# Optimization experiments

Measured on AMD Instinct MI355X. Metric: run time of the kernel, lower is better.

## Reference

```python
import jax, jax.numpy as jnp
import numpy as np

HEAD_NUM = 16

def setup_inputs() -> dict:
    key = jax.random.key(0)
    k1, k2 = jax.random.split(key)
    bs, seq, d = 2, 2048, 1024
    embeddings = jax.random.normal(k1, (bs, seq, d), dtype=jnp.float32)
    W = jax.random.normal(k2, (d, 3 * d), dtype=jnp.float32) * (1.0 / np.sqrt(d))
    b = jnp.zeros((3 * d,), dtype=jnp.float32)
    return {"embeddings": embeddings, "W": W, "b": b}

def reference(embeddings, W, b):
    bs, seq, d = embeddings.shape
    h = HEAD_NUM
    qkv = embeddings @ W + b                      # [b, s, 3d]
    q, k, v = jnp.split(qkv, 3, axis=-1)          # each [b, s, d]
    hd = d // h
    # Faithful to source: reshape to (bs, seq, head_dim, heads) then permute
    def split_heads(x, head_dim):
        return x.reshape(bs, seq, head_dim, h).transpose(0, 3, 1, 2)  # [b, h, s, hd]
    mq = split_heads(q, hd)
    mk = split_heads(k, hd)
    mv = split_heads(v, hd)
    scale = jnp.sqrt(jnp.asarray(hd, dtype=mq.dtype))
    scores = jnp.einsum('bhqd,bhkd->bhqk', mq, mk) / scale  # [b, h, s, s]
    attn = jax.nn.softmax(scores, axis=-1)
    out = jnp.einsum('bhqk,bhkv->bhqv', attn, mv)            # [b, h, s, hd]
    return out.transpose(0, 2, 1, 3).reshape(bs, seq, -1)    # [b, s, d]
```

## Files before the change

### kernel.cpp

```cpp
#include <hip/hip_runtime.h>
#include <stdint.h>

typedef unsigned short u16;
typedef unsigned int u32;
typedef float f32x4 __attribute__((ext_vector_type(4)));
typedef __bf16 bf16x8 __attribute__((ext_vector_type(8)));

#define BS 2
#define SEQ 2048
#define DIM 1024
#define NW3 3072
#define NH 16
#define HD 64

#define MFMA_BF16(a, b, c) __builtin_amdgcn_mfma_f32_16x16x32_bf16((a), (b), (c), 0, 0, 0)

#define GLL16(g, l)                                                                \
  __builtin_amdgcn_global_load_lds(                                                \
      (__attribute__((address_space(1))) void*)(void*)(uintptr_t)(g),              \
      (__attribute__((address_space(3))) void*)(l), 16, 0, 0)

__device__ __forceinline__ float fexp2(float x) {
#if defined(__has_builtin)
#if __has_builtin(__builtin_amdgcn_exp2f)
  return __builtin_amdgcn_exp2f(x);
#else
  return exp2f(x);
#endif
#else
  return exp2f(x);
#endif
}

__device__ __forceinline__ u16 f2bf(float x) {
  __bf16 h = (__bf16)x;
  return __builtin_bit_cast(u16, h);
}

#define CSC 0.18033688011112042f

__global__ __launch_bounds__(256) void conv_kernel(const float* __restrict__ A,
                                                   u16* __restrict__ O,
                                                   const float* __restrict__ W,
                                                   u16* __restrict__ Wt) {
  if (blockIdx.x < 4096) {
    int i = (blockIdx.x * 256 + threadIdx.x) * 4;
    float4 v = *(const float4*)(A + i);
    union { u16 u[4]; ushort4 v4; } p;
    p.u[0] = f2bf(v.x); p.u[1] = f2bf(v.y); p.u[2] = f2bf(v.z); p.u[3] = f2bf(v.w);
    *(ushort4*)(O + i) = p.v4;
  } else {
    int id = (blockIdx.x - 4096) * 256 + threadIdx.x;
    int kc = id / NW3;
    int n = id - kc * NW3;
    union { u16 u[8]; uint4 v; } p;
#pragma unroll
    for (int i = 0; i < 8; ++i) p.u[i] = f2bf(W[(kc * 8 + i) * NW3 + n]);
    int h = n & 15, hd = (n & 1023) >> 4;
    int np = (n & ~1023) + h * 64 + hd;
    *(uint4*)(Wt + np * DIM + kc * 8) = p.v;
  }
}

#define GSTAGE(ADST, BDST, KT)                                                 \
  {                                                                            \
    const int koff = (KT) * 64;                                \
    _Pragma("unroll") for (int r = 0; r < 2; ++r) {                            \
      int l = r * 256 + t;                            \
      int row = l >> 2, pos = l & 3;                                           \
      int kc = pos ^ (row & 3);                                                \
      GLL16(Abase + row * 2048 + koff + kc * 16, (char*)(ADST) + l * 16);      \
      GLL16(Bbase + row * 2048 + koff + kc * 16, (char*)(BDST) + l * 16);      \
    }                                                                          \
  }

#define GCOMPUTE(AT, BT)                                                       \
  {                                                                            \
    bf16x8 af[4], bfr[4];                                                      \
    _Pragma("unroll") for (int mt = 0; mt < 4; ++mt) {                         \
      int row = wm + mt * 16 + c;                                              \
      int kc = quad ^ (row & 3);                                               \
      af[mt] = *(const bf16x8*)((const char*)(AT) + row * 64 + kc * 16);       \
    }                                                                          \
    _Pragma("unroll") for (int nt = 0; nt < 4; ++nt) {                         \
      int row = wn + nt * 16 + c;                                              \
      int kc = quad ^ (row & 3);                                               \
      bfr[nt] = *(const bf16x8*)((const char*)(BT) + row * 64 + kc * 16);      \
    }                                                                          \
    _Pragma("unroll") for (int mt = 0; mt < 4; ++mt)                           \
      _Pragma("unroll") for (int nt = 0; nt < 4; ++nt)                         \
        acc[mt][nt] = MFMA_BF16(af[mt], bfr[nt], acc[mt][nt]);                 \
  }

__global__ __launch_bounds__(256) void gemm_qkv_kernel(
    const u16* __restrict__ Ab, const u16* __restrict__ Bt, const float* __restrict__ bias,
    u16* __restrict__ Q, u16* __restrict__ K, u16* __restrict__ Vt) {
  __shared__ __align__(16) u16 Aa[128 * 32];
  __shared__ __align__(16) u16 Ab2[128 * 32];
  __shared__ __align__(16) u16 Ba[128 * 32];
  __shared__ __align__(16) u16 Bb2[128 * 32];
  const int t = threadIdx.x;
  const int lane = t & 63, wave = t >> 6;
  const int c = lane & 15, quad = lane >> 4;
  const int tm = blockIdx.x / 24, tn = blockIdx.x - tm * 24;
  const int wm = (wave >> 1) * 64, wn = (wave & 1) * 64;

  const char* Abase = (const char*)(Ab + (size_t)tm * 128 * DIM);
  const char* Bbase = (const char*)(Bt + (size_t)tn * 128 * DIM);

  f32x4 z = {0.f, 0.f, 0.f, 0.f};
  f32x4 acc[4][4];
#pragma unroll
  for (int i = 0; i < 4; ++i)
#pragma unroll
    for (int j = 0; j < 4; ++j) acc[i][j] = z;

  GSTAGE(Aa, Ba, 0);
  __syncthreads();
  for (int kt = 0; kt < 32; kt += 2) {
    GSTAGE(Ab2, Bb2, kt + 1);
    GCOMPUTE(Aa, Ba);
    __syncthreads();
    if (kt + 2 < 32) GSTAGE(Aa, Ba, kt + 2);
    GCOMPUTE(Ab2, Bb2);
    __syncthreads();
  }

#pragma unroll
  for (int nt = 0; nt < 4; ++nt) {
    int np = tn * 128 + wn + nt * 16 + c;
    int which = np >> 10;
    int rem = np & 1023;
    int h = rem >> 6, hd = rem & 63;
    float bv = bias[(np & ~1023) + hd * 16 + h];
    float sc = (which == 0) ? CSC : 1.0f;
    float bvs = bv * sc;
#pragma unroll
    for (int mt = 0; mt < 4; ++mt) {
      int mbase = tm * 128 + wm + mt * 16 + quad * 4;
      int bI = mbase >> 11;
      int s0 = mbase & 2047;
      if (which == 2) {
        union { u16 u[4]; uint2 v; } p;
#pragma unroll
        for (int r = 0; r < 4; ++r) p.u[r] = f2bf(acc[mt][nt][r] + bv);
        *(uint2*)(Vt + ((size_t)(bI * NH + h) * HD + hd) * SEQ + s0) = p.v;
      } else {
        u16* dst = (which == 0) ? Q : K;
#pragma unroll
        for (int r = 0; r < 4; ++r)
          dst[((size_t)(bI * NH + h) * SEQ + (s0 + r)) * HD + hd] =
              f2bf(acc[mt][nt][r] * sc + bvs);
      }
    }
  }
}

#define STAGE_KV(KDST, VDST, KTILE)                                            \
  {                                                                            \
    const char* Ktb = Kb + (size_t)(KTILE) * 8192;        \
    const char* Vtb = Vb + (size_t)(KTILE) * 128;         \
    _Pragma("unroll") for (int r = 0; r < 2; ++r) {                            \
      int l = r * 256 + t;                                                     \
      int row = l >> 3, pos = l & 7;                                           \
      int kc = pos ^ (row & 7);                                                \
      GLL16(Ktb + row * 128 + kc * 16, (char*)(KDST) + l * 16);                \
      GLL16(Vtb + row * 4096 + kc * 16, (char*)(VDST) + l * 16);               \
    }                                                                          \
  }

#define COMPUTE_TILE(KT, VT)                                                   \
  {                                                                            \
    f32x4 sT[2][2]; \
    sT[0][0] = z; sT[0][1] = z; sT[1][0] = z; sT[1][1] = z;                    \
    _Pragma("unroll") for (int mt2 = 0; mt2 < 2; ++mt2) {                      \
      _Pragma("unroll") for (int ks = 0; ks < 2; ++ks) {                       \
        int row = ws * 32 + mt2 * 16 + c;                                      \
        int kc = (ks * 4 + quad) ^ (row & 7);                                  \
        bf16x8 kf = *(const bf16x8*)((const char*)(KT) + row * 128 + kc * 16); \
        sT[mt2][0] = MFMA_BF16(kf, qf[0][ks], sT[mt2][0]);                     \
        sT[mt2][1] = MFMA_BF16(kf, qf[1][ks], sT[mt2][1]);                     \
      }                                                                        \
    }                                                                          \
    bf16x8 pf[2];                                                              \
    _Pragma("unroll") for (int nt = 0; nt < 2; ++nt) {                         \
      u32 pk[2][2];                                                            \
      _Pragma("unroll") for (int mt2 = 0; mt2 < 2; ++mt2) {                    \
        float p0 = fexp2(sT[mt2][nt][0]);                                      \
        float p1 = fexp2(sT[mt2][nt][1]);                                      \
        float p2 = fexp2(sT[mt2][nt][2]);                                      \
        float p3 = fexp2(sT[mt2][nt][3]);                                      \
        smA[nt] += p0 + p1; smB[nt] += p2 + p3;                                \
        pk[mt2][0] = (u32)f2bf(p0) | ((u32)f2bf(p1) << 16);                    \
        pk[mt2][1] = (u32)f2bf(p2) | ((u32)f2bf(p3) << 16);                    \
      }                                                                        \
      u32 a0 = __shfl(pk[0][0], sl0), a1 = __shfl(pk[0][1], sl0);              \
      u32 a2 = __shfl(pk[0][0], sl1), a3 = __shfl(pk[0][1], sl1);              \
      u32 b0 = __shfl(pk[1][0], sl0), b1 = __shfl(pk[1][1], sl0);              \
      u32 b2 = __shfl(pk[1][0], sl1), b3 = __shfl(pk[1][1], sl1);              \
      uint4 wv;                                                                \
      wv.x = hi ? b0 : a0; wv.y = hi ? b1 : a1;                                \
      wv.z = hi ? b2 : a2; wv.w = hi ? b3 : a3;                                \
      pf[nt] = __builtin_bit_cast(bf16x8, wv);                                 \
    }                                                                          \
    _Pragma("unroll") for (int mt = 0; mt < 4; ++mt) {                         \
      int row = mt * 16 + c;                                                   \
      int kc = vq ^ (row & 7);                                                 \
      bf16x8 vf = *(const bf16x8*)((const char*)(VT) + row * 128 + kc * 16);   \
      accO[mt][0] = MFMA_BF16(vf, pf[0], accO[mt][0]);                         \
      accO[mt][1] = MFMA_BF16(vf, pf[1], accO[mt][1]);                         \
    }                                                                          \
  }

__global__ __launch_bounds__(256, 4) void attn_kernel(
    const u16* __restrict__ Q, const u16* __restrict__ K,
    const u16* __restrict__ Vt, float* __restrict__ Out) {
  __shared__ __align__(16) u16 Ka[64 * 64];
  __shared__ __align__(16) u16 Kb2[64 * 64];
  __shared__ __align__(16) u16 Va[64 * 64];
  __shared__ __align__(16) u16 Vb2[64 * 64];
  const int t = threadIdx.x;
  const int lane = t & 63, wave = t >> 6;
  const int c = lane & 15, quad = lane >> 4;
  const int wq = wave & 1, ws = wave >> 1;
  const int qt = blockIdx.x & 31, bh = blockIdx.x >> 5;
  const int h = bh & 15, b = bh >> 4;

  const u16* Qb = Q + ((size_t)bh * SEQ + qt * 64) * HD;
  const char* Kb = (const char*)(K + (size_t)bh * SEQ * HD);
  const char* Vb = (const char*)(Vt + (size_t)bh * HD * SEQ);

#pragma unroll
  for (int r = 0; r < 2; ++r) {
    int l = r * 256 + t;
    int row = l >> 3, pos = l & 7;
    int kc = pos ^ (row & 7);
    GLL16((const char*)Qb + row * 128 + kc * 16, (char*)Ka + l * 16);
  }
  __syncthreads();
  bf16x8 qf[2][2];
#pragma unroll
  for (int nt = 0; nt < 2; ++nt)
#pragma unroll
    for (int ks = 0; ks < 2; ++ks) {
      int row = wq * 32 + nt * 16 + c;
      int kc = (ks * 4 + quad) ^ (row & 7);
      qf[nt][ks] = *(const bf16x8*)((const char*)Ka + row * 128 + kc * 16);
    }
  __syncthreads();

  float smA[2] = {0.f, 0.f}, smB[2] = {0.f, 0.f};
  f32x4 z = {0.f, 0.f, 0.f, 0.f};
  f32x4 accO[4][2];
#pragma unroll
  for (int i = 0; i < 4; ++i) { accO[i][0] = z; accO[i][1] = z; }

  const int sl0 = c + 16 * ((quad & 1) * 2);
  const int sl1 = sl0 + 16;
  const bool hi = quad >= 2;
  const int vq = ws * 4 + quad;

  STAGE_KV(Ka, Va, 0);
  __syncthreads();

  for (int kt = 0; kt < 32; kt += 2) {
    STAGE_KV(Kb2, Vb2, kt + 1);
    COMPUTE_TILE(Ka, Va);
    __syncthreads();
    if (kt + 2 < 32) STAGE_KV(Ka, Va, kt + 2);
    COMPUTE_TILE(Kb2, Vb2);
    __syncthreads();
  }

  float sm[2];
#pragma unroll
  for (int nt = 0; nt < 2; ++nt) {
    float s = smA[nt] + smB[nt];
    s += __shfl_xor(s, 16);
    s += __shfl_xor(s, 32);
    sm[nt] = s;
  }
  if (ws == 1) {
    float* fb = (float*)(wq ? (void*)Kb2 : (void*)Ka);
#pragma unroll
    for (int mt = 0; mt < 4; ++mt)
#pragma unroll
      for (int nt = 0; nt < 2; ++nt)
        *(f32x4*)(fb + (mt * 2 + nt) * 256 + lane * 4) = accO[mt][nt];
    float* lb = (float*)Va + wq * 128;
    lb[lane * 2] = sm[0];
    lb[lane * 2 + 1] = sm[1];
  }
  __syncthreads();
  if (ws == 0) {
    const float* fb = (const float*)(wq ? (void*)Kb2 : (void*)Ka);
#pragma unroll
    for (int mt = 0; mt < 4; ++mt)
#pragma unroll
      for (int nt = 0; nt < 2; ++nt)
        accO[mt][nt] += *(const f32x4*)(fb + (mt * 2 + nt) * 256 + lane * 4);
    const float* lb = (const float*)Va + wq * 128;
    float inv0 = 1.f / (sm[0] + lb[lane * 2]);
    float inv1 = 1.f / (sm[1] + lb[lane * 2 + 1]);
    int s0 = qt * 64 + wq * 32 + c;
#pragma unroll
    for (int mt = 0; mt < 4; ++mt) {
#pragma unroll
      for (int nt = 0; nt < 2; ++nt) {
        float inv = nt ? inv1 : inv0;
        float4 o;
        o.x = accO[mt][nt][0] * inv;
        o.y = accO[mt][nt][1] * inv;
        o.z = accO[mt][nt][2] * inv;
        o.w = accO[mt][nt][3] * inv;
        size_t off = ((size_t)(b * SEQ + s0 + nt * 16)) * DIM + h * HD + mt * 16 + quad * 4;
        *(float4*)(Out + off) = o;
      }
    }
  }
}

extern "C" void kernel_launch(void* const* d_in, const int* in_sizes, int n_in,
                              void* d_out, int out_size, void* d_ws, size_t ws_size,
                              hipStream_t stream) {
  (void)in_sizes; (void)n_in; (void)out_size; (void)ws_size;
  const float* emb = (const float*)d_in[0];
  const float* W = (const float*)d_in[1];
  const float* bias = (const float*)d_in[2];
  float* out = (float*)d_out;
  char* ws = (char*)d_ws;
  u16* Ab = (u16*)ws;
  u16* Wt = (u16*)(ws + 8388608);
  u16* Qd = (u16*)(ws + 14680064);
  u16* Kd = (u16*)(ws + 23068672);
  u16* Vd = (u16*)(ws + 31457280);

  conv_kernel<<<5632, 256, 0, stream>>>(emb, Ab, W, Wt);
  gemm_qkv_kernel<<<768, 256, 0, stream>>>(Ab, Wt, bias, Qd, Kd, Vd);
  attn_kernel<<<1024, 256, 0, stream>>>(Qd, Kd, Vd, out);
}
```

Before: 175.6 us.

## Triple-buffer K/V tiles with one barrier per tile, XCD-aware block mapping, setprio

The attention loop moves from double-buffered K/V staging with two full syncthreads per tile pair to a rotating triple buffer. Loads run two tiles ahead and each tile waits on a partial vmcnt before a single barrier. Blocks are remapped so that all query tiles of a head land on the same XCD, so K/V reuse stays in that XCD's L2. MFMA sections are wrapped in s_setprio to favour matrix issue. The cost is 50% more LDS per block (24KB), which may limit occupancy, plus hand-tuned waitcnt values that must match the load counts exactly.

```diff
diff --git a/kernel.cpp b/kernel.cpp
--- a/kernel.cpp
+++ b/kernel.cpp
@@ -173,6 +173,7 @@
   {                                                                            \
     f32x4 sT[2][2]; \
     sT[0][0] = z; sT[0][1] = z; sT[1][0] = z; sT[1][1] = z;                    \
+    __builtin_amdgcn_s_setprio(1);                                             \
     _Pragma("unroll") for (int mt2 = 0; mt2 < 2; ++mt2) {                      \
       _Pragma("unroll") for (int ks = 0; ks < 2; ++ks) {                       \
         int row = ws * 32 + mt2 * 16 + c;                                      \
@@ -182,6 +183,7 @@
         sT[mt2][1] = MFMA_BF16(kf, qf[1][ks], sT[mt2][1]);                     \
       }                                                                        \
     }                                                                          \
+    __builtin_amdgcn_s_setprio(0);                                             \
     bf16x8 pf[2];                                                              \
     _Pragma("unroll") for (int nt = 0; nt < 2; ++nt) {                         \
       u32 pk[2][2];                                                            \
@@ -203,6 +205,7 @@
       wv.z = hi ? b2 : a2; wv.w = hi ? b3 : a3;                                \
       pf[nt] = __builtin_bit_cast(bf16x8, wv);                                 \
     }                                                                          \
+    __builtin_amdgcn_s_setprio(1);                                             \
     _Pragma("unroll") for (int mt = 0; mt < 4; ++mt) {                         \
       int row = mt * 16 + c;                                                   \
       int kc = vq ^ (row & 7);                                                 \
@@ -210,20 +213,26 @@
       accO[mt][0] = MFMA_BF16(vf, pf[0], accO[mt][0]);                         \
       accO[mt][1] = MFMA_BF16(vf, pf[1], accO[mt][1]);                         \
     }                                                                          \
+    __builtin_amdgcn_s_setprio(0);                                             \
   }
 
 __global__ __launch_bounds__(256, 4) void attn_kernel(
     const u16* __restrict__ Q, const u16* __restrict__ K,
     const u16* __restrict__ Vt, float* __restrict__ Out) {
-  __shared__ __align__(16) u16 Ka[64 * 64];
-  __shared__ __align__(16) u16 Kb2[64 * 64];
-  __shared__ __align__(16) u16 Va[64 * 64];
-  __shared__ __align__(16) u16 Vb2[64 * 64];
+  __shared__ __align__(16) u16 KB0[64 * 64];
+  __shared__ __align__(16) u16 KB1[64 * 64];
+  __shared__ __align__(16) u16 KB2[64 * 64];
+  __shared__ __align__(16) u16 VB0[64 * 64];
+  __shared__ __align__(16) u16 VB1[64 * 64];
+  __shared__ __align__(16) u16 VB2[64 * 64];
   const int t = threadIdx.x;
   const int lane = t & 63, wave = t >> 6;
   const int c = lane & 15, quad = lane >> 4;
   const int wq = wave & 1, ws = wave >> 1;
-  const int qt = blockIdx.x & 31, bh = blockIdx.x >> 5;
+  const int p = blockIdx.x;
+  const int xcd = p & 7, slot = p >> 3;
+  const int bh = xcd + ((slot >> 5) << 3);
+  const int qt = slot & 31;
   const int h = bh & 15, b = bh >> 4;
 
   const u16* Qb = Q + ((size_t)bh * SEQ + qt * 64) * HD;
@@ -235,9 +244,13 @@
     int l = r * 256 + t;
     int row = l >> 3, pos = l & 7;
     int kc = pos ^ (row & 7);
-    GLL16((const char*)Qb + row * 128 + kc * 16, (char*)Ka + l * 16);
-  }
-  __syncthreads();
+    GLL16((const char*)Qb + row * 128 + kc * 16, (char*)KB2 + l * 16);
+  }
+  STAGE_KV(KB0, VB0, 0);
+  STAGE_KV(KB1, VB1, 1);
+  asm volatile("s_waitcnt vmcnt(8)" ::: "memory");
+  __builtin_amdgcn_s_barrier();
+  __builtin_amdgcn_sched_barrier(0);
   bf16x8 qf[2][2];
 #pragma unroll
   for (int nt = 0; nt < 2; ++nt)
@@ -245,9 +258,11 @@
     for (int ks = 0; ks < 2; ++ks) {
       int row = wq * 32 + nt * 16 + c;
       int kc = (ks * 4 + quad) ^ (row & 7);
-      qf[nt][ks] = *(const bf16x8*)((const char*)Ka + row * 128 + kc * 16);
+      qf[nt][ks] = *(const bf16x8*)((const char*)KB2 + row * 128 + kc * 16);
     }
-  __syncthreads();
+  asm volatile("s_waitcnt vmcnt(4) lgkmcnt(0)" ::: "memory");
+  __builtin_amdgcn_s_barrier();
+  __builtin_amdgcn_sched_barrier(0);
 
   float smA[2] = {0.f, 0.f}, smB[2] = {0.f, 0.f};
   f32x4 z = {0.f, 0.f, 0.f, 0.f};
@@ -260,16 +275,22 @@
   const bool hi = quad >= 2;
   const int vq = ws * 4 + quad;
 
-  STAGE_KV(Ka, Va, 0);
-  __syncthreads();
-
-  for (int kt = 0; kt < 32; kt += 2) {
-    STAGE_KV(Kb2, Vb2, kt + 1);
-    COMPUTE_TILE(Ka, Va);
-    __syncthreads();
-    if (kt + 2 < 32) STAGE_KV(Ka, Va, kt + 2);
-    COMPUTE_TILE(Kb2, Vb2);
-    __syncthreads();
+  const u16 *ka = KB0, *va = VB0;
+  const u16 *kb2 = KB1, *vb2 = VB1;
+  const u16 *kc3 = KB2, *vc3 = VB2;
+#pragma unroll 1
+  for (int kt = 0; kt < 32; ++kt) {
+    if (kt + 2 < 32) STAGE_KV(kc3, vc3, kt + 2);
+    COMPUTE_TILE(ka, va);
+    if (kt + 2 < 32) {
+      asm volatile("s_waitcnt vmcnt(4)" ::: "memory");
+    } else {
+      asm volatile("s_waitcnt vmcnt(0)" ::: "memory");
+    }
+    __builtin_amdgcn_s_barrier();
+    __builtin_amdgcn_sched_barrier(0);
+    const u16* tk = ka; ka = kb2; kb2 = kc3; kc3 = tk;
+    const u16* tv = va; va = vb2; vb2 = vc3; vc3 = tv;
   }
 
   float sm[2];
@@ -281,25 +302,25 @@
     sm[nt] = s;
   }
   if (ws == 1) {
-    float* fb = (float*)(wq ? (void*)Kb2 : (void*)Ka);
+    float* fb = (float*)(wq ? (void*)KB1 : (void*)KB0);
 #pragma unroll
     for (int mt = 0; mt < 4; ++mt)
 #pragma unroll
       for (int nt = 0; nt < 2; ++nt)
         *(f32x4*)(fb + (mt * 2 + nt) * 256 + lane * 4) = accO[mt][nt];
-    float* lb = (float*)Va + wq * 128;
+    float* lb = (float*)VB0 + wq * 128;
     lb[lane * 2] = sm[0];
     lb[lane * 2 + 1] = sm[1];
   }
   __syncthreads();
   if (ws == 0) {
-    const float* fb = (const float*)(wq ? (void*)Kb2 : (void*)Ka);
+    const float* fb = (const float*)(wq ? (void*)KB1 : (void*)KB0);
 #pragma unroll
     for (int mt = 0; mt < 4; ++mt)
 #pragma unroll
       for (int nt = 0; nt < 2; ++nt)
         accO[mt][nt] += *(const f32x4*)(fb + (mt * 2 + nt) * 256 + lane * 4);
-    const float* lb = (const float*)Va + wq * 128;
+    const float* lb = (const float*)VB0 + wq * 128;
     float inv0 = 1.f / (sm[0] + lb[lane * 2]);
     float inv1 = 1.f / (sm[1] + lb[lane * 2 + 1]);
     int s0 = qt * 64 + wq * 32 + c;
```

Measured after the change: 185.0 us. 1.05x slower.
